# Kernel tuning notes

Hardware: AMD Instinct MI355X
Metric: run time of the kernel (lower is better)

Reference implementation:

```python
import jax, jax.numpy as jnp
import numpy as np

N = 4096      # num_nodes
D_IN = 768    # input_dim
HID = 512     # hidden_dim per head
D_OUT = 768   # output_dim
H = 4         # num_heads
ALPHA = 0.2   # LeakyReLU slope
NEG_BIG = -9e15


def _layer_norm(x, g, b, eps=1e-5):
    m = jnp.mean(x, axis=-1, keepdims=True)
    v = jnp.var(x, axis=-1, keepdims=True)
    return (x - m) * jax.lax.rsqrt(v + eps) * g + b


def _multihead_gat(h, mask, ew, W, a, concat):
    # h: [N, F_in], W: [H, F_in, O], a: [H, 2*O], mask/ew: [N, N]
    O = W.shape[-1]
    Wh = jnp.einsum('nf,hfo->hno', h, W)                      # [H, N, O]
    # e[h,i,j] = leakyrelu(a1.Wh[i] + a2.Wh[j]) -- equivalent to the
    # concat(Wh_i, Wh_j) @ a formulation, without the O(N^2 * 2O) tensor.
    s_src = jnp.einsum('hno,ho->hn', Wh, a[:, :O])            # [H, N]
    s_dst = jnp.einsum('hno,ho->hn', Wh, a[:, O:])            # [H, N]
    e = jax.nn.leaky_relu(s_src[:, :, None] + s_dst[:, None, :], negative_slope=ALPHA)
    att = jnp.where(mask[None], e, NEG_BIG)
    if ew is not None:
        att = att * ew[None]                                   # faithful: scale AFTER masking
    att = jax.nn.softmax(att, axis=-1)                         # dropout is identity at eval
    hp = jnp.einsum('hnm,hmo->hno', att, Wh)                   # [H, N, O]
    if concat:
        return jax.nn.elu(jnp.transpose(hp, (1, 0, 2)).reshape(h.shape[0], H * O))
    return jnp.mean(hp, axis=0)                                # concat=False: mean, no ELU


def setup_inputs() -> dict:
    key = jax.random.key(0)
    ks = jax.random.split(key, 10)
    return {
        'node_features': jax.random.normal(ks[0], (N, D_IN), jnp.float32),
        'adjacency': jax.random.randint(ks[1], (N, N), 0, 2, jnp.int32),
        'edge_weights': jax.random.uniform(ks[2], (N, N), jnp.float32),
        'W0': (jax.random.normal(ks[3], (H, D_IN, HID)) * 0.05).astype(jnp.float32),
        'a0': (jax.random.normal(ks[4], (H, 2 * HID)) * 0.05).astype(jnp.float32),
        'W1': (jax.random.normal(ks[5], (H, HID * H, D_OUT)) * 0.02).astype(jnp.float32),
        'a1': (jax.random.normal(ks[6], (H, 2 * D_OUT)) * 0.05).astype(jnp.float32),
        'rp0_w': (jax.random.normal(ks[7], (D_IN, HID * H)) * 0.02).astype(jnp.float32),
        'rp0_b': jnp.zeros((HID * H,), jnp.float32),
        'rp1_w': (jax.random.normal(ks[8], (HID * H, D_OUT)) * 0.02).astype(jnp.float32),
        'rp1_b': jnp.zeros((D_OUT,), jnp.float32),
        'ln0_g': jnp.ones((HID * H,), jnp.float32),
        'ln0_b': jnp.zeros((HID * H,), jnp.float32),
        'ln1_g': jnp.ones((D_OUT,), jnp.float32),
        'ln1_b': jnp.zeros((D_OUT,), jnp.float32),
    }


def reference(node_features, adjacency, edge_weights, W0, a0, W1, a1,
              rp0_w, rp0_b, rp1_w, rp1_b, ln0_g, ln0_b, ln1_g, ln1_b):
    n = node_features.shape[0]
    adj = adjacency.astype(jnp.float32) + jnp.eye(n, dtype=jnp.float32)  # add self-loops
    mask = adj > 0
    h = node_features
    # layer 0: concat heads -> [N, H*HID], residual projection, LN, ELU (dropout=identity)
    h1 = _multihead_gat(h, mask, edge_weights, W0, a0, concat=True)
    h1 = h1 + (h @ rp0_w + rp0_b)
    h1 = _layer_norm(h1, ln0_g, ln0_b)
    h1 = jax.nn.elu(h1)
    # layer 1 (last): mean over heads -> [N, D_OUT], residual projection, LN
    h2 = _multihead_gat(h1, mask, edge_weights, W1, a1, concat=False)
    h2 = h2 + (h1 @ rp1_w + rp1_b)
    h2 = _layer_norm(h2, ln1_g, ln1_b)
    return h2
```

## Files before the change

### kernel.cpp

```cpp
#include <hip/hip_runtime.h>


typedef unsigned short u16;
typedef unsigned char u8;
typedef unsigned long long u64;
using short8  = __attribute__((ext_vector_type(8))) short;
using float4v = __attribute__((ext_vector_type(4))) float;
using int4v   = __attribute__((ext_vector_type(4))) int;
using int8v   = __attribute__((ext_vector_type(8))) int;

#define NN 4096
#define NHEADS 4

__device__ __forceinline__ u16 f2bf(float f) {
  union { float f; unsigned u; } v; v.f = f;
  unsigned u = v.u;
  return (u16)((u + 0x7FFFu + ((u >> 16) & 1u)) >> 16);
}
__device__ __forceinline__ float bf2f(u16 x) {
  union { unsigned u; float f; } v; v.u = ((unsigned)x) << 16; return v.f;
}
__device__ __forceinline__ unsigned pk_fp8x4(float a, float b, float c, float d) {
  int lo = __builtin_amdgcn_cvt_pk_fp8_f32(a, b, 0, false);
  return (unsigned)__builtin_amdgcn_cvt_pk_fp8_f32(c, d, lo, true);
}

__device__ __forceinline__ void async16(const void* g, void* l) {
  __builtin_amdgcn_global_load_lds(
      (const __attribute__((address_space(1))) unsigned int*)g,
      (__attribute__((address_space(3))) unsigned int*)l, 16, 0, 0);
}

__global__ __launch_bounds__(256) void cast_f32_bf16(const float* __restrict__ in,
                                                     u16* __restrict__ out, int n) {
  int i = blockIdx.x * 256 + threadIdx.x;
  if (i < n) out[i] = f2bf(in[i]);
}

__global__ __launch_bounds__(256) void adj2bits(const int* __restrict__ adj,
                                                u64* __restrict__ bits) {
  size_t gw = (size_t)blockIdx.x * 4 + (threadIdx.x >> 6);
  int lane = threadIdx.x & 63;
  int v = adj[gw * 64 + lane];
  u64 b = __ballot(v != 0);
  if (lane == 0) bits[gw] = b;
}

__global__ __launch_bounds__(256) void transcast_f32(const float* __restrict__ in,
                                                     u16* __restrict__ out, int R, int C) {
  __shared__ float t[32][33];
  size_t zoff = (size_t)blockIdx.z * R * C;
  in += zoff; out += zoff;
  int c0 = blockIdx.x * 32, r0 = blockIdx.y * 32;
  int tx = threadIdx.x & 31, ty = threadIdx.x >> 5;
#pragma unroll
  for (int i = 0; i < 32; i += 8)
    t[ty + i][tx] = in[(size_t)(r0 + ty + i) * C + (c0 + tx)];
  __syncthreads();
#pragma unroll
  for (int i = 0; i < 32; i += 8)
    out[(size_t)(c0 + ty + i) * R + (r0 + tx)] = f2bf(t[tx][ty + i]);
}

__global__ __launch_bounds__(256) void wa_kernel(const float* __restrict__ W,
                                                 const float* __restrict__ a,
                                                 float* __restrict__ wa, int F, int O) {
  int gw = blockIdx.x * 4 + (threadIdx.x >> 6);
  int lane = threadIdx.x & 63;
  int total = 2 * NHEADS * F;
  if (gw >= total) return;
  int side = gw / (NHEADS * F);
  int rem = gw - side * NHEADS * F;
  int h = rem / F, f = rem - h * F;
  const float* wrow = W + ((size_t)h * F + f) * O;
  const float* av = a + (size_t)h * 2 * O + (size_t)side * O;
  float s = 0.f;
  for (int o = lane; o < O; o += 64) s += wrow[o] * av[o];
#pragma unroll
  for (int off = 32; off > 0; off >>= 1) s += __shfl_down(s, off);
  if (lane == 0) wa[gw] = s;
}

__global__ __launch_bounds__(256) void s8_kernel_f32(const float* __restrict__ X,
                                                     const float* __restrict__ wa,
                                                     float* __restrict__ sout, int F) {
  int n = blockIdx.x * 4 + (threadIdx.x >> 6);
  int lane = threadIdx.x & 63;
  const float* x = X + (size_t)n * F;
  float acc[8] = {};
  for (int f = lane; f < F; f += 64) {
    float xv = x[f];
#pragma unroll
    for (int k = 0; k < 8; k++) acc[k] += xv * wa[(size_t)k * F + f];
  }
#pragma unroll
  for (int k = 0; k < 8; k++) {
    float s = acc[k];
#pragma unroll
    for (int off = 32; off > 0; off >>= 1) s += __shfl_down(s, off);
    if (lane == 0) sout[(size_t)k * NN + n] = s;
  }
}

__global__ __launch_bounds__(256) void s8_kernel_bf16(const u16* __restrict__ X,
                                                      const float* __restrict__ wa,
                                                      float* __restrict__ sout, int F) {
  int n = blockIdx.x * 4 + (threadIdx.x >> 6);
  int lane = threadIdx.x & 63;
  const u16* x = X + (size_t)n * F;
  float acc[8] = {};
  for (int f = lane; f < F; f += 64) {
    float xv = bf2f(x[f]);
#pragma unroll
    for (int k = 0; k < 8; k++) acc[k] += xv * wa[(size_t)k * F + f];
  }
#pragma unroll
  for (int k = 0; k < 8; k++) {
    float s = acc[k];
#pragma unroll
    for (int off = 32; off > 0; off >>= 1) s += __shfl_down(s, off);
    if (lane == 0) sout[(size_t)k * NN + n] = s;
  }
}

__global__ __launch_bounds__(256) void sdmax_kernel(const float* __restrict__ s,
                                                    float* __restrict__ out) {
  int h = blockIdx.x, tid = threadIdx.x;
  const float* sd = s + (size_t)(NHEADS + h) * NN;
  float m = -3e38f;
  for (int i = tid; i < NN; i += 256) m = fmaxf(m, sd[i]);
  __shared__ float red[4];
#pragma unroll
  for (int off = 32; off > 0; off >>= 1) m = fmaxf(m, __shfl_down(m, off));
  if ((tid & 63) == 0) red[tid >> 6] = m;
  __syncthreads();
  if (tid == 0) out[h] = fmaxf(fmaxf(red[0], red[1]), fmaxf(red[2], red[3]));
}

template <int G>
__global__ __launch_bounds__(256) void pexp_g_kernel(const u64* __restrict__ mb,
                                                     const float* __restrict__ ew,
                                                     const float* __restrict__ s,
                                                     const float* __restrict__ sdmax,
                                                     u8* __restrict__ P,
                                                     float* __restrict__ L, int hb) {
  __shared__ u64 mrow[64];
  __shared__ float lred[G][4];
  int i = blockIdx.x, tid = threadIdx.x;
  if (tid < 64) mrow[tid] = mb[(size_t)i * 64 + tid];
  float sr[G], mp[G], lacc[G];
#pragma unroll
  for (int z = 0; z < G; z++) {
    sr[z] = s[(size_t)(hb + z) * NN + i];
    mp[z] = fmaxf(0.0f, sr[z] + sdmax[hb + z]);
    lacc[z] = 0.f;
  }
  const float4* wrow = (const float4*)(ew + (size_t)i * NN);
  __syncthreads();
  for (int jv = tid; jv < NN / 4; jv += 256) {
    float4 w = wrow[jv];
    int j0 = jv * 4;
    u64 mw = mrow[jv >> 4] >> (j0 & 63);
    float we[4]; we[0] = w.x; we[1] = w.y; we[2] = w.z; we[3] = w.w;
    bool m[4];
#pragma unroll
    for (int k = 0; k < 4; k++) m[k] = ((mw >> k) & 1ull) || (j0 + k == i);
#pragma unroll
    for (int z = 0; z < G; z++) {
      const float4 sd4 = *(const float4*)(s + (size_t)(NHEADS + hb + z) * NN + j0);
      float sd[4]; sd[0] = sd4.x; sd[1] = sd4.y; sd[2] = sd4.z; sd[3] = sd4.w;
      float p[4];
#pragma unroll
      for (int k = 0; k < 4; k++) {
        float x = sr[z] + sd[k];
        float e = x > 0.f ? x : 0.2f * x;
        float v = (m[k] ? e : -9e15f) * we[k];
        p[k] = __expf(v - mp[z]);
        lacc[z] += p[k];
      }
      *(unsigned*)(P + ((size_t)z * NN + i) * NN + j0) = pk_fp8x4(p[0], p[1], p[2], p[3]);
    }
  }
#pragma unroll
  for (int z = 0; z < G; z++) {
    float r = lacc[z];
#pragma unroll
    for (int off = 32; off > 0; off >>= 1) r += __shfl_down(r, off);
    if ((tid & 63) == 0) lred[z][tid >> 6] = r;
  }
  __syncthreads();
  if (tid < G)
    L[(size_t)(hb + tid) * NN + i] = lred[tid][0] + lred[tid][1] + lred[tid][2] + lred[tid][3];
}

__global__ __launch_bounds__(256) void gemm_proj(const u16* __restrict__ A,
                                                 const u16* __restrict__ Bt,
                                                 u8* __restrict__ F8T,
                                                 float* __restrict__ F32,
                                                 const float* __restrict__ bias,
                                                 int K, int split, int ldcF) {
  int row0 = blockIdx.x * 128;
  int col0 = blockIdx.y * 128;

  __shared__ u16 ldsA[128 * 64];
  __shared__ u16 ldsB[128 * 64];

  int tid = threadIdx.x;
  int wave = tid >> 6, lane = tid & 63;
  int wm = wave >> 1, wn = wave & 1;
  int lm = lane & 15, quad = lane >> 4;

  int sr = tid >> 3, sc = tid & 7;
  int scg = sc ^ (sr & 7);
  const u16* aPtr = A  + (size_t)(row0 + sr) * K + scg * 8;
  const u16* bPtr = Bt + (size_t)(col0 + sr) * K + scg * 8;
  u16* ldsAw = &ldsA[wave * 512];
  u16* ldsBw = &ldsB[wave * 512];
  const size_t rowStep = (size_t)32 * K;

  float4v acc[4][4] = {};

  for (int k0 = 0; k0 < K; k0 += 64) {
    __syncthreads();
#pragma unroll
    for (int b = 0; b < 4; b++) {
      async16(aPtr + k0 + b * rowStep, ldsAw + b * 2048);
      async16(bPtr + k0 + b * rowStep, ldsBw + b * 2048);
    }
    __syncthreads();
    short8 af[4][2], bf[4][2];
#pragma unroll
    for (int s = 0; s < 4; s++) {
      int ra = wm * 64 + s * 16 + lm;
      int rb = wn * 64 + s * 16 + lm;
      int swa = ra & 7, swb = rb & 7;
      af[s][0] = *(const short8*)(&ldsA[ra * 64 + ((quad ^ swa) * 8)]);
      af[s][1] = *(const short8*)(&ldsA[ra * 64 + (((4 + quad) ^ swa) * 8)]);
      bf[s][0] = *(const short8*)(&ldsB[rb * 64 + ((quad ^ swb) * 8)]);
      bf[s][1] = *(const short8*)(&ldsB[rb * 64 + (((4 + quad) ^ swb) * 8)]);
    }
#pragma unroll
    for (int i = 0; i < 4; i++)
#pragma unroll
      for (int j = 0; j < 4; j++) {
        acc[i][j] = __builtin_amdgcn_mfma_f32_16x16x32_bf16(af[i][0], bf[j][0], acc[i][j], 0, 0, 0);
        acc[i][j] = __builtin_amdgcn_mfma_f32_16x16x32_bf16(af[i][1], bf[j][1], acc[i][j], 0, 0, 0);
      }
  }

  if (col0 < split) {
#pragma unroll
    for (int i = 0; i < 4; i++) {
#pragma unroll
      for (int j = 0; j < 4; j++) {
        int grow0 = row0 + wm * 64 + i * 16 + (lane >> 4) * 4;
        int gcol = col0 + wn * 64 + j * 16 + lm;
        unsigned pk = pk_fp8x4(acc[i][j][0], acc[i][j][1], acc[i][j][2], acc[i][j][3]);
        *(unsigned*)&F8T[(size_t)gcol * NN + grow0] = pk;
      }
    }
  } else {
#pragma unroll
    for (int i = 0; i < 4; i++) {
#pragma unroll
      for (int j = 0; j < 4; j++) {
#pragma unroll
        for (int r = 0; r < 4; r++) {
          int grow = row0 + wm * 64 + i * 16 + (lane >> 4) * 4 + r;
          int gcol = col0 + wn * 64 + j * 16 + lm - split;
          F32[(size_t)grow * ldcF + gcol] = acc[i][j][r] + bias[gcol];
        }
      }
    }
  }
}

template <int MODE>
__global__ __launch_bounds__(256) void gemm_mx(const u8* __restrict__ A,
                                               const u8* __restrict__ Bt,
                                               float* __restrict__ Cout,
                                               int ldc, int coloff_base, int coloff_step,
                                               size_t bStride, size_t cStride) {
  constexpr int K = NN;
  int h = blockIdx.z;
  const u8* Ab = A + (size_t)h * ((size_t)NN * NN);
  const u8* Bb = Bt + (size_t)h * bStride;
  int row0 = blockIdx.x * 128;
  int col0 = blockIdx.y * 128;
  int coloff = coloff_base + h * coloff_step;

  __shared__ u8 ldsA[128 * 128];
  __shared__ u8 ldsB[128 * 128];

  int tid = threadIdx.x;
  int wave = tid >> 6, lane = tid & 63;
  int wm = wave >> 1, wn = wave & 1;
  int lm = lane & 15, quad = lane >> 4;

  int sr = tid >> 3, sc = tid & 7;
  int scg = sc ^ (sr & 7);
  const u8* aPtr = Ab + (size_t)(row0 + sr) * K + scg * 16;
  const u8* bPtr = Bb + (size_t)(col0 + sr) * K + scg * 16;
  u8* ldsAw = &ldsA[wave * 1024];
  u8* ldsBw = &ldsB[wave * 1024];
  const size_t rowStep = (size_t)32 * K;

  float4v acc[4][4] = {};

  for (int k0 = 0; k0 < K; k0 += 128) {
    __syncthreads();
#pragma unroll
    for (int b = 0; b < 4; b++) {
      async16(aPtr + k0 + b * rowStep, ldsAw + b * 4096);
      async16(bPtr + k0 + b * rowStep, ldsBw + b * 4096);
    }
    __syncthreads();
    int8v a32[4], b32[4];
#pragma unroll
    for (int s = 0; s < 4; s++) {
      int ra = wm * 64 + s * 16 + lm;
      int rb = wn * 64 + s * 16 + lm;
      int swa = ra & 7, swb = rb & 7;
      int4v alo = *(const int4v*)(&ldsA[ra * 128 + (((2 * quad) ^ swa) * 16)]);
      int4v ahi = *(const int4v*)(&ldsA[ra * 128 + (((2 * quad + 1) ^ swa) * 16)]);
      int4v blo = *(const int4v*)(&ldsB[rb * 128 + (((2 * quad) ^ swb) * 16)]);
      int4v bhi = *(const int4v*)(&ldsB[rb * 128 + (((2 * quad + 1) ^ swb) * 16)]);
      a32[s][0] = alo[0]; a32[s][1] = alo[1]; a32[s][2] = alo[2]; a32[s][3] = alo[3];
      a32[s][4] = ahi[0]; a32[s][5] = ahi[1]; a32[s][6] = ahi[2]; a32[s][7] = ahi[3];
      b32[s][0] = blo[0]; b32[s][1] = blo[1]; b32[s][2] = blo[2]; b32[s][3] = blo[3];
      b32[s][4] = bhi[0]; b32[s][5] = bhi[1]; b32[s][6] = bhi[2]; b32[s][7] = bhi[3];
    }
#pragma unroll
    for (int i = 0; i < 4; i++)
#pragma unroll
      for (int j = 0; j < 4; j++)
        acc[i][j] = __builtin_amdgcn_mfma_scale_f32_16x16x128_f8f6f4(
            a32[i], b32[j], acc[i][j], 0, 0, 0, 127, 0, 127);
  }

#pragma unroll
  for (int i = 0; i < 4; i++) {
#pragma unroll
    for (int j = 0; j < 4; j++) {
#pragma unroll
      for (int r = 0; r < 4; r++) {
        int grow = row0 + wm * 64 + i * 16 + quad * 4 + r;
        int gcol = col0 + wn * 64 + j * 16 + lm;
        float v = acc[i][j][r];
        if constexpr (MODE == 2) {
          Cout[(size_t)grow * ldc + coloff + gcol] = v;
        } else {
          Cout[(size_t)h * cStride + (size_t)grow * ldc + gcol] = v;
        }
      }
    }
  }
}

__global__ __launch_bounds__(256) void ln0_kernel(const float* __restrict__ accin,
                                                  const float* __restrict__ rp,
                                                  const float* __restrict__ Lsum,
                                                  const float* __restrict__ g,
                                                  const float* __restrict__ b,
                                                  u16* __restrict__ h1b) {
  const int C = 2048;
  int n = blockIdx.x, tid = threadIdx.x;
  __shared__ float xs[2048];
  __shared__ float red[2][4];
  __shared__ float mrs[2];
  float linv[NHEADS];
#pragma unroll
  for (int h = 0; h < NHEADS; h++) linv[h] = 1.0f / Lsum[(size_t)h * NN + n];
  float sum = 0.f, sq = 0.f;
  const float* ar = accin + (size_t)n * C;
  const float* rr = rp + (size_t)n * C;
  for (int c = tid; c < C; c += 256) {
    float v = ar[c] * linv[c >> 9];
    v = v > 0.f ? v : (__expf(v) - 1.f);
    float x = v + rr[c];
    xs[c] = x; sum += x; sq += x * x;
  }
#pragma unroll
  for (int off = 32; off > 0; off >>= 1) { sum += __shfl_down(sum, off); sq += __shfl_down(sq, off); }
  if ((tid & 63) == 0) { red[0][tid >> 6] = sum; red[1][tid >> 6] = sq; }
  __syncthreads();
  if (tid == 0) {
    float s = red[0][0] + red[0][1] + red[0][2] + red[0][3];
    float q = red[1][0] + red[1][1] + red[1][2] + red[1][3];
    float mean = s / C, var = q / C - mean * mean;
    mrs[0] = mean; mrs[1] = rsqrtf(var + 1e-5f);
  }
  __syncthreads();
  float mean = mrs[0], rstd = mrs[1];
  for (int c = tid; c < C; c += 256) {
    float y = (xs[c] - mean) * rstd * g[c] + b[c];
    float z = y > 0.f ? y : (__expf(y) - 1.f);
    h1b[(size_t)n * C + c] = f2bf(z);
  }
}

__global__ __launch_bounds__(256) void ln1_kernel(const float* __restrict__ hp1,
                                                  const float* __restrict__ rp1,
                                                  const float* __restrict__ Lsum,
                                                  const float* __restrict__ g,
                                                  const float* __restrict__ b,
                                                  float* __restrict__ out) {
  const int C = 768;
  int n = blockIdx.x, tid = threadIdx.x;
  __shared__ float xs[768];
  __shared__ float red[2][4];
  __shared__ float mrs[2];
  float linv[NHEADS];
#pragma unroll
  for (int h = 0; h < NHEADS; h++) linv[h] = 0.25f / Lsum[(size_t)h * NN + n];
  float sum = 0.f, sq = 0.f;
  for (int c = tid; c < C; c += 256) {
    float x = hp1[((size_t)0 * NN + n) * C + c] * linv[0] +
              hp1[((size_t)1 * NN + n) * C + c] * linv[1] +
              hp1[((size_t)2 * NN + n) * C + c] * linv[2] +
              hp1[((size_t)3 * NN + n) * C + c] * linv[3];
    x += rp1[(size_t)n * C + c];
    xs[c] = x; sum += x; sq += x * x;
  }
#pragma unroll
  for (int off = 32; off > 0; off >>= 1) { sum += __shfl_down(sum, off); sq += __shfl_down(sq, off); }
  if ((tid & 63) == 0) { red[0][tid >> 6] = sum; red[1][tid >> 6] = sq; }
  __syncthreads();
  if (tid == 0) {
    float s = red[0][0] + red[0][1] + red[0][2] + red[0][3];
    float q = red[1][0] + red[1][1] + red[1][2] + red[1][3];
    float mean = s / C, var = q / C - mean * mean;
    mrs[0] = mean; mrs[1] = rsqrtf(var + 1e-5f);
  }
  __syncthreads();
  float mean = mrs[0], rstd = mrs[1];
  for (int c = tid; c < C; c += 256)
    out[(size_t)n * C + c] = (xs[c] - mean) * rstd * g[c] + b[c];
}

extern "C" void kernel_launch(void* const* d_in, const int* in_sizes, int n_in,
                              void* d_out, int out_size, void* d_ws, size_t ws_size,
                              hipStream_t stream) {
  (void)in_sizes; (void)n_in; (void)out_size;
  const float* X    = (const float*)d_in[0];
  const int*   adj  = (const int*)d_in[1];
  const float* ew   = (const float*)d_in[2];
  const float* W0   = (const float*)d_in[3];
  const float* a0   = (const float*)d_in[4];
  const float* W1   = (const float*)d_in[5];
  const float* a1   = (const float*)d_in[6];
  const float* rp0w = (const float*)d_in[7];
  const float* rp0b = (const float*)d_in[8];
  const float* rp1w = (const float*)d_in[9];
  const float* rp1b = (const float*)d_in[10];
  const float* ln0g = (const float*)d_in[11];
  const float* ln0b = (const float*)d_in[12];
  const float* ln1g = (const float*)d_in[13];
  const float* ln1b = (const float*)d_in[14];
  float* out = (float*)d_out;
  char* wsb = (char*)d_ws;

  constexpr size_t OFF_XBF   = 0;
  constexpr size_t OFF_W0T   = 6291456;
  constexpr size_t OFF_RP0WT = 9437184;
  constexpr size_t OFF_W1T   = 12582912;
  constexpr size_t OFF_RP1WT = 25165824;
  constexpr size_t OFF_WA0   = 28311552;
  constexpr size_t OFF_WA1   = 28336128;
  constexpr size_t OFF_S0    = 28401664;
  constexpr size_t OFF_S1    = 28532736;
  constexpr size_t OFF_L0    = 28664320;
  constexpr size_t OFF_L1    = 28729856;
  constexpr size_t OFF_H1B   = 28795392;
  constexpr size_t D         = 45572608;
  constexpr size_t PD        = D + 50331648;
  constexpr size_t PN        = (size_t)NN * NN;
  constexpr size_t OFF_HP1   = PD + 4 * PN;
  constexpr size_t OFF_MASK  = 213344768;
  constexpr size_t OFF_SM0   = 215441920;
  constexpr size_t OFF_SM1   = 215442176;

  u16*   XBF   = (u16*)(wsb + OFF_XBF);
  u16*   W0T   = (u16*)(wsb + OFF_W0T);
  u16*   RP0WT = (u16*)(wsb + OFF_RP0WT);
  u16*   W1T   = (u16*)(wsb + OFF_W1T);
  u16*   RP1WT = (u16*)(wsb + OFF_RP1WT);
  float* WA0   = (float*)(wsb + OFF_WA0);
  float* WA1   = (float*)(wsb + OFF_WA1);
  float* S0    = (float*)(wsb + OFF_S0);
  float* S1    = (float*)(wsb + OFF_S1);
  float* L0    = (float*)(wsb + OFF_L0);
  float* L1    = (float*)(wsb + OFF_L1);
  u16*   H1B   = (u16*)(wsb + OFF_H1B);
  u8*    WH0T  = (u8*)(wsb + D);
  float* RP0   = (float*)(wsb + D + 16777216);
  u8*    WH1T  = (u8*)(wsb + D);
  float* RP1   = (float*)(wsb + D + 25165824);
  u8*    P     = (u8*)(wsb + PD);
  float* HP1   = (float*)(wsb + OFF_HP1);
  float* ACC0  = (float*)(wsb + OFF_HP1);
  u64*   MASK  = (u64*)(wsb + OFF_MASK);
  float* SM0   = (float*)(wsb + OFF_SM0);
  float* SM1   = (float*)(wsb + OFF_SM1);

  const int G = (ws_size >= OFF_HP1 + 50331648) ? 4 : 1;

  adj2bits<<<dim3(65536), 256, 0, stream>>>(adj, MASK);
  cast_f32_bf16<<<dim3((NN * 768 + 255) / 256), 256, 0, stream>>>(X, XBF, NN * 768);
  transcast_f32<<<dim3(16, 24, 4), 256, 0, stream>>>(W0, W0T, 768, 512);
  transcast_f32<<<dim3(24, 64, 4), 256, 0, stream>>>(W1, W1T, 2048, 768);
  transcast_f32<<<dim3(64, 24, 1), 256, 0, stream>>>(rp0w, RP0WT, 768, 2048);
  transcast_f32<<<dim3(24, 64, 1), 256, 0, stream>>>(rp1w, RP1WT, 2048, 768);

  wa_kernel<<<dim3(2 * NHEADS * 768 / 4), 256, 0, stream>>>(W0, a0, WA0, 768, 512);
  s8_kernel_f32<<<dim3(NN / 4), 256, 0, stream>>>(X, WA0, S0, 768);
  sdmax_kernel<<<dim3(NHEADS), 256, 0, stream>>>(S0, SM0);

  gemm_proj<<<dim3(32, 32), 256, 0, stream>>>(XBF, W0T, WH0T, RP0, rp0b, 768, 2048, 2048);

  for (int g = 0; g < NHEADS; g += G) {
    if (G == 4) pexp_g_kernel<4><<<dim3(NN), 256, 0, stream>>>(MASK, ew, S0, SM0, P, L0, g);
    else        pexp_g_kernel<1><<<dim3(NN), 256, 0, stream>>>(MASK, ew, S0, SM0, P, L0, g);
    gemm_mx<2><<<dim3(32, 4, G), 256, 0, stream>>>(P, WH0T + (size_t)g * 512 * NN,
        ACC0, 2048, g * 512, 512, (size_t)512 * NN, 0);
  }
  ln0_kernel<<<dim3(NN), 256, 0, stream>>>(ACC0, RP0, L0, ln0g, ln0b, H1B);

  wa_kernel<<<dim3(2 * NHEADS * 2048 / 4), 256, 0, stream>>>(W1, a1, WA1, 2048, 768);
  s8_kernel_bf16<<<dim3(NN / 4), 256, 0, stream>>>(H1B, WA1, S1, 2048);
  sdmax_kernel<<<dim3(NHEADS), 256, 0, stream>>>(S1, SM1);

  gemm_proj<<<dim3(32, 30), 256, 0, stream>>>(H1B, W1T, WH1T, RP1, rp1b, 2048, 3072, 768);

  for (int g = 0; g < NHEADS; g += G) {
    if (G == 4) pexp_g_kernel<4><<<dim3(NN), 256, 0, stream>>>(MASK, ew, S1, SM1, P, L1, g);
    else        pexp_g_kernel<1><<<dim3(NN), 256, 0, stream>>>(MASK, ew, S1, SM1, P, L1, g);
    gemm_mx<3><<<dim3(32, 6, G), 256, 0, stream>>>(P, WH1T + (size_t)g * 768 * NN,
        HP1 + (size_t)g * NN * 768, 768, 0, 0, (size_t)768 * NN, (size_t)NN * 768);
  }
  ln1_kernel<<<dim3(NN), 256, 0, stream>>>(HP1, RP1, L1, ln1g, ln1b, out);
}
```

Baseline: 642.2 us.

## Merge projection GEMM and attention-exp into one heterogeneous launch, fuse small prologues

The projection GEMM and the masked exp/fp8 P-matrix computation become a single kernel. Block IDs are interleaved so that every fifth block runs a GEMM tile and the rest compute one attention row, letting the compute-bound and bandwidth-bound work overlap on the GPU. The f32→bf16 cast is folded into the layer-0 score kernel, and the layer-1 score dot products move into the LayerNorm-0 epilogue, which removes separate passes over X and H1. The fallback that processed one head per launch when the workspace was small is removed, so the code now assumes enough workspace for all four heads.

```diff
diff --git a/kernel.cpp b/kernel.cpp
--- a/kernel.cpp
+++ b/kernel.cpp
@@ -24,17 +24,10 @@
   int lo = __builtin_amdgcn_cvt_pk_fp8_f32(a, b, 0, false);
   return (unsigned)__builtin_amdgcn_cvt_pk_fp8_f32(c, d, lo, true);
 }
-
 __device__ __forceinline__ void async16(const void* g, void* l) {
   __builtin_amdgcn_global_load_lds(
       (const __attribute__((address_space(1))) unsigned int*)g,
       (__attribute__((address_space(3))) unsigned int*)l, 16, 0, 0);
-}
-
-__global__ __launch_bounds__(256) void cast_f32_bf16(const float* __restrict__ in,
-                                                     u16* __restrict__ out, int n) {
-  int i = blockIdx.x * 256 + threadIdx.x;
-  if (i < n) out[i] = f2bf(in[i]);
 }
 
 __global__ __launch_bounds__(256) void adj2bits(const int* __restrict__ adj,
@@ -81,36 +74,18 @@
   if (lane == 0) wa[gw] = s;
 }
 
-__global__ __launch_bounds__(256) void s8_kernel_f32(const float* __restrict__ X,
-                                                     const float* __restrict__ wa,
-                                                     float* __restrict__ sout, int F) {
+__global__ __launch_bounds__(256) void cast_s8_f32(const float* __restrict__ X,
+                                                   const float* __restrict__ wa,
+                                                   u16* __restrict__ XBF,
+                                                   float* __restrict__ sout, int F) {
   int n = blockIdx.x * 4 + (threadIdx.x >> 6);
   int lane = threadIdx.x & 63;
   const float* x = X + (size_t)n * F;
+  u16* xb = XBF + (size_t)n * F;
   float acc[8] = {};
   for (int f = lane; f < F; f += 64) {
     float xv = x[f];
-#pragma unroll
-    for (int k = 0; k < 8; k++) acc[k] += xv * wa[(size_t)k * F + f];
-  }
-#pragma unroll
-  for (int k = 0; k < 8; k++) {
-    float s = acc[k];
-#pragma unroll
-    for (int off = 32; off > 0; off >>= 1) s += __shfl_down(s, off);
-    if (lane == 0) sout[(size_t)k * NN + n] = s;
-  }
-}
-
-__global__ __launch_bounds__(256) void s8_kernel_bf16(const u16* __restrict__ X,
-                                                      const float* __restrict__ wa,
-                                                      float* __restrict__ sout, int F) {
-  int n = blockIdx.x * 4 + (threadIdx.x >> 6);
-  int lane = threadIdx.x & 63;
-  const u16* x = X + (size_t)n * F;
-  float acc[8] = {};
-  for (int f = lane; f < F; f += 64) {
-    float xv = bf2f(x[f]);
+    xb[f] = f2bf(xv);
 #pragma unroll
     for (int k = 0; k < 8; k++) acc[k] += xv * wa[(size_t)k * F + f];
   }
@@ -137,141 +112,144 @@
   if (tid == 0) out[h] = fmaxf(fmaxf(red[0], red[1]), fmaxf(red[2], red[3]));
 }
 
-template <int G>
-__global__ __launch_bounds__(256) void pexp_g_kernel(const u64* __restrict__ mb,
-                                                     const float* __restrict__ ew,
-                                                     const float* __restrict__ s,
-                                                     const float* __restrict__ sdmax,
-                                                     u8* __restrict__ P,
-                                                     float* __restrict__ L, int hb) {
-  __shared__ u64 mrow[64];
-  __shared__ float lred[G][4];
-  int i = blockIdx.x, tid = threadIdx.x;
-  if (tid < 64) mrow[tid] = mb[(size_t)i * 64 + tid];
-  float sr[G], mp[G], lacc[G];
-#pragma unroll
-  for (int z = 0; z < G; z++) {
-    sr[z] = s[(size_t)(hb + z) * NN + i];
-    mp[z] = fmaxf(0.0f, sr[z] + sdmax[hb + z]);
-    lacc[z] = 0.f;
-  }
-  const float4* wrow = (const float4*)(ew + (size_t)i * NN);
-  __syncthreads();
-  for (int jv = tid; jv < NN / 4; jv += 256) {
-    float4 w = wrow[jv];
-    int j0 = jv * 4;
-    u64 mw = mrow[jv >> 4] >> (j0 & 63);
-    float we[4]; we[0] = w.x; we[1] = w.y; we[2] = w.z; we[3] = w.w;
-    bool m[4];
-#pragma unroll
-    for (int k = 0; k < 4; k++) m[k] = ((mw >> k) & 1ull) || (j0 + k == i);
-#pragma unroll
-    for (int z = 0; z < G; z++) {
-      const float4 sd4 = *(const float4*)(s + (size_t)(NHEADS + hb + z) * NN + j0);
-      float sd[4]; sd[0] = sd4.x; sd[1] = sd4.y; sd[2] = sd4.z; sd[3] = sd4.w;
-      float p[4];
-#pragma unroll
-      for (int k = 0; k < 4; k++) {
-        float x = sr[z] + sd[k];
-        float e = x > 0.f ? x : 0.2f * x;
-        float v = (m[k] ? e : -9e15f) * we[k];
-        p[k] = __expf(v - mp[z]);
-        lacc[z] += p[k];
-      }
-      *(unsigned*)(P + ((size_t)z * NN + i) * NN + j0) = pk_fp8x4(p[0], p[1], p[2], p[3]);
-    }
-  }
-#pragma unroll
-  for (int z = 0; z < G; z++) {
-    float r = lacc[z];
-#pragma unroll
-    for (int off = 32; off > 0; off >>= 1) r += __shfl_down(r, off);
-    if ((tid & 63) == 0) lred[z][tid >> 6] = r;
-  }
-  __syncthreads();
-  if (tid < G)
-    L[(size_t)(hb + tid) * NN + i] = lred[tid][0] + lred[tid][1] + lred[tid][2] + lred[tid][3];
-}
-
-__global__ __launch_bounds__(256) void gemm_proj(const u16* __restrict__ A,
+__global__ __launch_bounds__(256) void proj_pexp(const u16* __restrict__ A,
                                                  const u16* __restrict__ Bt,
                                                  u8* __restrict__ F8T,
                                                  float* __restrict__ F32,
                                                  const float* __restrict__ bias,
-                                                 int K, int split, int ldcF) {
-  int row0 = blockIdx.x * 128;
-  int col0 = blockIdx.y * 128;
-
+                                                 int K, int split, int ldcF, int nproj,
+                                                 const u64* __restrict__ mb,
+                                                 const float* __restrict__ ew,
+                                                 const float* __restrict__ s,
+                                                 const float* __restrict__ sdmax,
+                                                 u8* __restrict__ P,
+                                                 float* __restrict__ L) {
   __shared__ u16 ldsA[128 * 64];
   __shared__ u16 ldsB[128 * 64];
-
+  __shared__ u64 mrow[64];
+  __shared__ float lred[4][4];
+
+  int bid = blockIdx.x;
+  int q = bid / 5;
   int tid = threadIdx.x;
-  int wave = tid >> 6, lane = tid & 63;
-  int wm = wave >> 1, wn = wave & 1;
-  int lm = lane & 15, quad = lane >> 4;
-
-  int sr = tid >> 3, sc = tid & 7;
-  int scg = sc ^ (sr & 7);
-  const u16* aPtr = A  + (size_t)(row0 + sr) * K + scg * 8;
-  const u16* bPtr = Bt + (size_t)(col0 + sr) * K + scg * 8;
-  u16* ldsAw = &ldsA[wave * 512];
-  u16* ldsBw = &ldsB[wave * 512];
-  const size_t rowStep = (size_t)32 * K;
-
-  float4v acc[4][4] = {};
-
-  for (int k0 = 0; k0 < K; k0 += 64) {
-    __syncthreads();
-#pragma unroll
-    for (int b = 0; b < 4; b++) {
-      async16(aPtr + k0 + b * rowStep, ldsAw + b * 2048);
-      async16(bPtr + k0 + b * rowStep, ldsBw + b * 2048);
-    }
-    __syncthreads();
-    short8 af[4][2], bf[4][2];
-#pragma unroll
-    for (int s = 0; s < 4; s++) {
-      int ra = wm * 64 + s * 16 + lm;
-      int rb = wn * 64 + s * 16 + lm;
-      int swa = ra & 7, swb = rb & 7;
-      af[s][0] = *(const short8*)(&ldsA[ra * 64 + ((quad ^ swa) * 8)]);
-      af[s][1] = *(const short8*)(&ldsA[ra * 64 + (((4 + quad) ^ swa) * 8)]);
-      bf[s][0] = *(const short8*)(&ldsB[rb * 64 + ((quad ^ swb) * 8)]);
-      bf[s][1] = *(const short8*)(&ldsB[rb * 64 + (((4 + quad) ^ swb) * 8)]);
-    }
-#pragma unroll
-    for (int i = 0; i < 4; i++)
-#pragma unroll
-      for (int j = 0; j < 4; j++) {
-        acc[i][j] = __builtin_amdgcn_mfma_f32_16x16x32_bf16(af[i][0], bf[j][0], acc[i][j], 0, 0, 0);
-        acc[i][j] = __builtin_amdgcn_mfma_f32_16x16x32_bf16(af[i][1], bf[j][1], acc[i][j], 0, 0, 0);
+
+  if ((bid % 5 == 0) && (q < nproj)) {
+    int row0 = (q & 31) * 128;
+    int col0 = (q >> 5) * 128;
+    int wave = tid >> 6, lane = tid & 63;
+    int wm = wave >> 1, wn = wave & 1;
+    int lm = lane & 15, quad = lane >> 4;
+
+    int sr = tid >> 3, sc = tid & 7;
+    int scg = sc ^ (sr & 7);
+    const u16* aPtr = A  + (size_t)(row0 + sr) * K + scg * 8;
+    const u16* bPtr = Bt + (size_t)(col0 + sr) * K + scg * 8;
+    u16* ldsAw = &ldsA[wave * 512];
+    u16* ldsBw = &ldsB[wave * 512];
+    const size_t rowStep = (size_t)32 * K;
+
+    float4v acc[4][4] = {};
+
+    for (int k0 = 0; k0 < K; k0 += 64) {
+      __syncthreads();
+#pragma unroll
+      for (int b = 0; b < 4; b++) {
+        async16(aPtr + k0 + b * rowStep, ldsAw + b * 2048);
+        async16(bPtr + k0 + b * rowStep, ldsBw + b * 2048);
       }
-  }
-
-  if (col0 < split) {
-#pragma unroll
-    for (int i = 0; i < 4; i++) {
-#pragma unroll
-      for (int j = 0; j < 4; j++) {
-        int grow0 = row0 + wm * 64 + i * 16 + (lane >> 4) * 4;
-        int gcol = col0 + wn * 64 + j * 16 + lm;
-        unsigned pk = pk_fp8x4(acc[i][j][0], acc[i][j][1], acc[i][j][2], acc[i][j][3]);
-        *(unsigned*)&F8T[(size_t)gcol * NN + grow0] = pk;
+      __syncthreads();
+      short8 af[4][2], bf[4][2];
+#pragma unroll
+      for (int ss = 0; ss < 4; ss++) {
+        int ra = wm * 64 + ss * 16 + lm;
+        int rb = wn * 64 + ss * 16 + lm;
+        int swa = ra & 7, swb = rb & 7;
+        af[ss][0] = *(const short8*)(&ldsA[ra * 64 + ((quad ^ swa) * 8)]);
+        af[ss][1] = *(const short8*)(&ldsA[ra * 64 + (((4 + quad) ^ swa) * 8)]);
+        bf[ss][0] = *(const short8*)(&ldsB[rb * 64 + ((quad ^ swb) * 8)]);
+        bf[ss][1] = *(const short8*)(&ldsB[rb * 64 + (((4 + quad) ^ swb) * 8)]);
       }
-    }
-  } else {
-#pragma unroll
-    for (int i = 0; i < 4; i++) {
-#pragma unroll
-      for (int j = 0; j < 4; j++) {
-#pragma unroll
-        for (int r = 0; r < 4; r++) {
-          int grow = row0 + wm * 64 + i * 16 + (lane >> 4) * 4 + r;
-          int gcol = col0 + wn * 64 + j * 16 + lm - split;
-          F32[(size_t)grow * ldcF + gcol] = acc[i][j][r] + bias[gcol];
+#pragma unroll
+      for (int i = 0; i < 4; i++)
+#pragma unroll
+        for (int j = 0; j < 4; j++) {
+          acc[i][j] = __builtin_amdgcn_mfma_f32_16x16x32_bf16(af[i][0], bf[j][0], acc[i][j], 0, 0, 0);
+          acc[i][j] = __builtin_amdgcn_mfma_f32_16x16x32_bf16(af[i][1], bf[j][1], acc[i][j], 0, 0, 0);
+        }
+    }
+
+    if (col0 < split) {
+#pragma unroll
+      for (int i = 0; i < 4; i++) {
+#pragma unroll
+        for (int j = 0; j < 4; j++) {
+          int grow0 = row0 + wm * 64 + i * 16 + quad * 4;
+          int gcol = col0 + wn * 64 + j * 16 + lm;
+          unsigned pk = pk_fp8x4(acc[i][j][0], acc[i][j][1], acc[i][j][2], acc[i][j][3]);
+          *(unsigned*)&F8T[(size_t)gcol * NN + grow0] = pk;
         }
       }
-    }
+    } else {
+#pragma unroll
+      for (int i = 0; i < 4; i++) {
+#pragma unroll
+        for (int j = 0; j < 4; j++) {
+#pragma unroll
+          for (int r = 0; r < 4; r++) {
+            int grow = row0 + wm * 64 + i * 16 + quad * 4 + r;
+            int gcol = col0 + wn * 64 + j * 16 + lm - split;
+            F32[(size_t)grow * ldcF + gcol] = acc[i][j][r] + bias[gcol];
+          }
+        }
+      }
+    }
+  } else {
+    int cnt = q + 1; if (cnt > nproj) cnt = nproj;
+    int i = bid - cnt;
+    if (tid < 64) mrow[tid] = mb[(size_t)i * 64 + tid];
+    float srh[4], mp[4], lacc[4];
+#pragma unroll
+    for (int z = 0; z < 4; z++) {
+      srh[z] = s[(size_t)z * NN + i];
+      mp[z] = fmaxf(0.0f, srh[z] + sdmax[z]);
+      lacc[z] = 0.f;
+    }
+    const float4* wrow = (const float4*)(ew + (size_t)i * NN);
+    __syncthreads();
+    for (int jv = tid; jv < NN / 4; jv += 256) {
+      float4 w = wrow[jv];
+      int j0 = jv * 4;
+      u64 mw = mrow[jv >> 4] >> (j0 & 63);
+      float we[4]; we[0] = w.x; we[1] = w.y; we[2] = w.z; we[3] = w.w;
+      bool m[4];
+#pragma unroll
+      for (int k = 0; k < 4; k++) m[k] = ((mw >> k) & 1ull) || (j0 + k == i);
+#pragma unroll
+      for (int z = 0; z < 4; z++) {
+        const float4 sd4 = *(const float4*)(s + (size_t)(NHEADS + z) * NN + j0);
+        float sd[4]; sd[0] = sd4.x; sd[1] = sd4.y; sd[2] = sd4.z; sd[3] = sd4.w;
+        float p[4];
+#pragma unroll
+        for (int k = 0; k < 4; k++) {
+          float x = srh[z] + sd[k];
+          float e = x > 0.f ? x : 0.2f * x;
+          float v = (m[k] ? e : -9e15f) * we[k];
+          p[k] = __expf(v - mp[z]);
+          lacc[z] += p[k];
+        }
+        *(unsigned*)(P + ((size_t)z * NN + i) * NN + j0) = pk_fp8x4(p[0], p[1], p[2], p[3]);
+      }
+    }
+#pragma unroll
+    for (int z = 0; z < 4; z++) {
+      float r = lacc[z];
+#pragma unroll
+      for (int off = 32; off > 0; off >>= 1) r += __shfl_down(r, off);
+      if ((tid & 63) == 0) lred[z][tid >> 6] = r;
+    }
+    __syncthreads();
+    if (tid < 4)
+      L[(size_t)tid * NN + i] = lred[tid][0] + lred[tid][1] + lred[tid][2] + lred[tid][3];
   }
 }
 
@@ -362,11 +340,14 @@
                                                   const float* __restrict__ Lsum,
                                                   const float* __restrict__ g,
                                                   const float* __restrict__ b,
-                                                  u16* __restrict__ h1b) {
+                                                  const float* __restrict__ wa1,
+                                                  u16* __restrict__ h1b,
+                                                  float* __restrict__ S1out) {
   const int C = 2048;
   int n = blockIdx.x, tid = threadIdx.x;
   __shared__ float xs[2048];
   __shared__ float red[2][4];
+  __shared__ float red8[8][4];
   __shared__ float mrs[2];
   float linv[NHEADS];
 #pragma unroll
@@ -392,11 +373,26 @@
   }
   __syncthreads();
   float mean = mrs[0], rstd = mrs[1];
+  float acc8[8] = {};
   for (int c = tid; c < C; c += 256) {
     float y = (xs[c] - mean) * rstd * g[c] + b[c];
     float z = y > 0.f ? y : (__expf(y) - 1.f);
-    h1b[(size_t)n * C + c] = f2bf(z);
-  }
+    u16 zr = f2bf(z);
+    h1b[(size_t)n * C + c] = zr;
+    float zb = bf2f(zr);
+#pragma unroll
+    for (int k = 0; k < 8; k++) acc8[k] += zb * wa1[(size_t)k * C + c];
+  }
+#pragma unroll
+  for (int k = 0; k < 8; k++) {
+    float s = acc8[k];
+#pragma unroll
+    for (int off = 32; off > 0; off >>= 1) s += __shfl_down(s, off);
+    if ((tid & 63) == 0) red8[k][tid >> 6] = s;
+  }
+  __syncthreads();
+  if (tid < 8)
+    S1out[(size_t)tid * NN + n] = red8[tid][0] + red8[tid][1] + red8[tid][2] + red8[tid][3];
 }
 
 __global__ __launch_bounds__(256) void ln1_kernel(const float* __restrict__ hp1,
@@ -441,7 +437,7 @@
 extern "C" void kernel_launch(void* const* d_in, const int* in_sizes, int n_in,
                               void* d_out, int out_size, void* d_ws, size_t ws_size,
                               hipStream_t stream) {
-  (void)in_sizes; (void)n_in; (void)out_size;
+  (void)in_sizes; (void)n_in; (void)out_size; (void)ws_size;
   const float* X    = (const float*)d_in[0];
   const int*   adj  = (const int*)d_in[1];
   const float* ew   = (const float*)d_in[2];
@@ -503,40 +499,26 @@
   float* SM0   = (float*)(wsb + OFF_SM0);
   float* SM1   = (float*)(wsb + OFF_SM1);
 
-  const int G = (ws_size >= OFF_HP1 + 50331648) ? 4 : 1;
-
   adj2bits<<<dim3(65536), 256, 0, stream>>>(adj, MASK);
-  cast_f32_bf16<<<dim3((NN * 768 + 255) / 256), 256, 0, stream>>>(X, XBF, NN * 768);
+  wa_kernel<<<dim3(2 * NHEADS * 768 / 4), 256, 0, stream>>>(W0, a0, WA0, 768, 512);
+  wa_kernel<<<dim3(2 * NHEADS * 2048 / 4), 256, 0, stream>>>(W1, a1, WA1, 2048, 768);
+  cast_s8_f32<<<dim3(NN / 4), 256, 0, stream>>>(X, WA0, XBF, S0, 768);
+  sdmax_kernel<<<dim3(NHEADS), 256, 0, stream>>>(S0, SM0);
   transcast_f32<<<dim3(16, 24, 4), 256, 0, stream>>>(W0, W0T, 768, 512);
   transcast_f32<<<dim3(24, 64, 4), 256, 0, stream>>>(W1, W1T, 2048, 768);
   transcast_f32<<<dim3(64, 24, 1), 256, 0, stream>>>(rp0w, RP0WT, 768, 2048);
   transcast_f32<<<dim3(24, 64, 1), 256, 0, stream>>>(rp1w, RP1WT, 2048, 768);
 
-  wa_kernel<<<dim3(2 * NHEADS * 768 / 4), 256, 0, stream>>>(W0, a0, WA0, 768, 512);
-  s8_kernel_f32<<<dim3(NN / 4), 256, 0, stream>>>(X, WA0, S0, 768);
-  sdmax_kernel<<<dim3(NHEADS), 256, 0, stream>>>(S0, SM0);
-
-  gemm_proj<<<dim3(32, 32), 256, 0, stream>>>(XBF, W0T, WH0T, RP0, rp0b, 768, 2048, 2048);
-
-  for (int g = 0; g < NHEADS; g += G) {
-    if (G == 4) pexp_g_kernel<4><<<dim3(NN), 256, 0, stream>>>(MASK, ew, S0, SM0, P, L0, g);
-    else        pexp_g_kernel<1><<<dim3(NN), 256, 0, stream>>>(MASK, ew, S0, SM0, P, L0, g);
-    gemm_mx<2><<<dim3(32, 4, G), 256, 0, stream>>>(P, WH0T + (size_t)g * 512 * NN,
-        ACC0, 2048, g * 512, 512, (size_t)512 * NN, 0);
-  }
-  ln0_kernel<<<dim3(NN), 256, 0, stream>>>(ACC0, RP0, L0, ln0g, ln0b, H1B);
-
-  wa_kernel<<<dim3(2 * NHEADS * 2048 / 4), 256, 0, stream>>>(W1, a1, WA1, 2048, 768);
-  s8_kernel_bf16<<<dim3(NN / 4), 256, 0, stream>>>(H1B, WA1, S1, 2048);
+  proj_pexp<<<dim3(1024 + 4096), 256, 0, stream>>>(XBF, W0T, WH0T, RP0, rp0b,
+      768, 2048, 2048, 1024, MASK, ew, S0, SM0, P, L0);
+  gemm_mx<2><<<dim3(32, 4, 4), 256, 0, stream>>>(P, WH0T, ACC0, 2048, 0, 512,
+      (size_t)512 * NN, 0);
+  ln0_kernel<<<dim3(NN), 256, 0, stream>>>(ACC0, RP0, L0, ln0g, ln0b, WA1, H1B, S1);
   sdmax_kernel<<<dim3(NHEADS), 256, 0, stream>>>(S1, SM1);
 
-  gemm_proj<<<dim3(32, 30), 256, 0, stream>>>(H1B, W1T, WH1T, RP1, rp1b, 2048, 3072, 768);
-
-  for (int g = 0; g < NHEADS; g += G) {
-    if (G == 4) pexp_g_kernel<4><<<dim3(NN), 256, 0, stream>>>(MASK, ew, S1, SM1, P, L1, g);
-    else        pexp_g_kernel<1><<<dim3(NN), 256, 0, stream>>>(MASK, ew, S1, SM1, P, L1, g);
-    gemm_mx<3><<<dim3(32, 6, G), 256, 0, stream>>>(P, WH1T + (size_t)g * 768 * NN,
-        HP1 + (size_t)g * NN * 768, 768, 0, 0, (size_t)768 * NN, (size_t)NN * 768);
-  }
+  proj_pexp<<<dim3(960 + 4096), 256, 0, stream>>>(H1B, W1T, WH1T, RP1, rp1b,
+      2048, 3072, 768, 960, MASK, ew, S1, SM1, P, L1);
+  gemm_mx<3><<<dim3(32, 6, 4), 256, 0, stream>>>(P, WH1T, HP1, 768, 0, 0,
+      (size_t)768 * NN, (size_t)NN * 768);
   ln1_kernel<<<dim3(NN), 256, 0, stream>>>(HP1, RP1, L1, ln1g, ln1b, out);
 }
```

Result: slower. 681.0 us (+6.0%).
